# Performance work log

Measured on AMD Instinct MI355X. Metric: run time of the kernel, lower is better.

## Reference

```python
import jax, jax.numpy as jnp
import numpy as np

B, S, D, H = 2, 2048, 1024, 16
DK = D // H  # 64
NEG_FILL = -1e-08  # faithful to the original (NOT -1e9)


def setup_inputs() -> dict:
    key = jax.random.key(0)
    ks = jax.random.split(key, 11)
    init = 1.0 / np.sqrt(D)
    inp = {
        "Q": jax.random.normal(ks[0], (B, S, D), jnp.float32),
        "K": jax.random.normal(ks[1], (B, S, D), jnp.float32),
        "V": jax.random.normal(ks[2], (B, S, D), jnp.float32),
        # causal mask, broadcast over batch and heads
        "mask": jnp.tril(jnp.ones((1, 1, S, S), jnp.int32)),
        "Wq": jax.random.normal(ks[3], (D, D), jnp.float32) * init,
        "bq": jnp.zeros((D,), jnp.float32),
        "Wk": jax.random.normal(ks[4], (D, D), jnp.float32) * init,
        "bk": jnp.zeros((D,), jnp.float32),
        "Wv": jax.random.normal(ks[5], (D, D), jnp.float32) * init,
        "bv": jnp.zeros((D,), jnp.float32),
        "Wo": jax.random.normal(ks[6], (D, D), jnp.float32) * init,
        "bo": jnp.zeros((D,), jnp.float32),
    }
    return inp


def reference(Q, K, V, mask, Wq, bq, Wk, bk, Wv, bv, Wo, bo):
    # Linear projections (weights stored as [in, out]; same math as nn.Linear)
    q = Q @ Wq + bq  # [B,S,D]
    k = K @ Wk + bk
    v = V @ Wv + bv
    # split heads: [B,S,D] -> [B,H,S,DK]
    q = q.reshape(B, S, H, DK).transpose(0, 2, 1, 3)
    k = k.reshape(B, S, H, DK).transpose(0, 2, 1, 3)
    v = v.reshape(B, S, H, DK).transpose(0, 2, 1, 3)
    scores = jnp.einsum("bhqd,bhkd->bhqk", q, k) / np.sqrt(DK)  # [B,H,S,S]
    scores = jnp.where(mask == 0, NEG_FILL, scores)
    probs = jax.nn.softmax(scores, axis=-1)
    # dropout p=0.0 -> identity (deterministic baseline)
    ctx = jnp.einsum("bhqk,bhkd->bhqd", probs, v)  # [B,H,S,DK]
    ctx = ctx.transpose(0, 2, 1, 3).reshape(B, S, D)
    return ctx @ Wo + bo
```

## Files before the change

kernel.cpp:

```cpp
#include <hip/hip_runtime.h>
#include <hip/hip_bf16.h>
#include <stdint.h>
#include <math.h>

#define DI __device__ __forceinline__

typedef __bf16 bf16x8 __attribute__((ext_vector_type(8)));
typedef float f32x4 __attribute__((ext_vector_type(4)));
typedef unsigned short ushortx8 __attribute__((ext_vector_type(8)));

DI unsigned short f2bf(float f) {
    unsigned int u = __builtin_bit_cast(unsigned int, f);
    u += 0x7fffu + ((u >> 16) & 1u);
    return (unsigned short)(u >> 16);
}

DI unsigned int cvt_pk_bf16(float lo, float hi) {
    unsigned int r;
    asm("v_cvt_pk_bf16_f32 %0, %1, %2" : "=v"(r) : "v"(lo), "v"(hi));
    return r;
}

DI f32x4 mfma_16x16x32_bf16(bf16x8 a, bf16x8 b, f32x4 c) {
    return __builtin_amdgcn_mfma_f32_16x16x32_bf16(a, b, c, 0, 0, 0);
}

DI void gload16(const unsigned short* g, unsigned short* l) {
    __builtin_amdgcn_global_load_lds(
        (const __attribute__((address_space(1))) void*)g,
        (__attribute__((address_space(3))) void*)l, 16, 0, 0);
}

__global__ __launch_bounds__(256) void k_prep(
    const float* __restrict__ Q, const float* __restrict__ K, const float* __restrict__ V,
    unsigned short* __restrict__ qc, unsigned short* __restrict__ kc, unsigned short* __restrict__ vc,
    const float* __restrict__ w0, const float* __restrict__ w1,
    const float* __restrict__ w2, const float* __restrict__ w3,
    unsigned short* __restrict__ o0, unsigned short* __restrict__ o1,
    unsigned short* __restrict__ o2, unsigned short* __restrict__ o3)
{
    constexpr int N = 1024;
    __shared__ unsigned short L[64 * 64];
    const int bx = blockIdx.x;
    const int tid = threadIdx.x;

    if (bx < 3072) {
        const int z = bx >> 10;
        const int ib = bx & 1023;
        const float* s = z == 0 ? Q : z == 1 ? K : V;
        unsigned short* d = z == 0 ? qc : z == 1 ? kc : vc;
        const int i0 = ib * 256 + tid;
        #pragma unroll
        for (int it = 0; it < 4; ++it) {
            const int i = i0 + it * 262144;
            const float4 v = reinterpret_cast<const float4*>(s)[i];
            uint2 pk;
            pk.x = cvt_pk_bf16(v.x, v.y);
            pk.y = cvt_pk_bf16(v.z, v.w);
            reinterpret_cast<uint2*>(d)[i] = pk;
        }
    } else {
        const int r4 = bx - 3072;
        const int z = r4 >> 8;
        const int tile = r4 & 255;
        const float* W = z == 0 ? w0 : z == 1 ? w1 : z == 2 ? w2 : w3;
        unsigned short* O = z == 0 ? o0 : z == 1 ? o1 : z == 2 ? o2 : o3;
        const int k0 = (tile >> 4) * 64, n0 = (tile & 15) * 64;

        const int r = tid >> 2, cbase = (tid & 3) * 16;
        #pragma unroll
        for (int i = 0; i < 4; ++i) {
            const int c = cbase + i * 4;
            const float4 v = *reinterpret_cast<const float4*>(&W[(size_t)(k0 + r) * N + n0 + c]);
            uint2 pk;
            pk.x = cvt_pk_bf16(v.x, v.y);
            pk.y = cvt_pk_bf16(v.z, v.w);
            const int byte = r * 128 + ((c * 2) ^ ((r & 7) << 4));
            *reinterpret_cast<uint2*>(reinterpret_cast<char*>(L) + byte) = pk;
        }
        __syncthreads();

        const int n = tid >> 2, kc2 = (tid & 3) * 16;
        ushortx8 v0, v1;
        #pragma unroll
        for (int j = 0; j < 8; ++j) {
            const int ka = kc2 + j, kb2 = kc2 + 8 + j;
            v0[j] = *reinterpret_cast<const unsigned short*>(
                reinterpret_cast<const char*>(L) + ka * 128 + ((n * 2) ^ ((ka & 7) << 4)));
            v1[j] = *reinterpret_cast<const unsigned short*>(
                reinterpret_cast<const char*>(L) + kb2 * 128 + ((n * 2) ^ ((kb2 & 7) << 4)));
        }
        unsigned short* op = &O[(size_t)(n0 + n) * N + k0 + kc2];
        *reinterpret_cast<ushortx8*>(op) = v0;
        *reinterpret_cast<ushortx8*>(op + 8) = v1;
    }
}

template <int MODE, int BN>
__global__ __launch_bounds__(256) void k_gemm_bf16(
    const unsigned short* __restrict__ A0, const unsigned short* __restrict__ A1,
    const unsigned short* __restrict__ A2,
    const unsigned short* __restrict__ B0, const unsigned short* __restrict__ B1,
    const unsigned short* __restrict__ B2,
    const float* __restrict__ bias0, const float* __restrict__ bias1,
    const float* __restrict__ bias2,
    void* C0, void* C1, void* C2)
{
    constexpr int K = 1024, N = 1024;
    constexpr int NJ = BN / 32;
    const int z = MODE ? blockIdx.z : 0;
    const unsigned short* A  = z == 0 ? A0 : z == 1 ? A1 : A2;
    const unsigned short* Bt = z == 0 ? B0 : z == 1 ? B1 : B2;
    const float* bias        = z == 0 ? bias0 : z == 1 ? bias1 : bias2;
    void* C                  = z == 0 ? C0 : z == 1 ? C1 : C2;

    __shared__ unsigned short As[128 * 64];
    __shared__ unsigned short Bs[BN * 64];

    const int tid  = threadIdx.x;
    const int lane = tid & 63;
    const int w    = tid >> 6;
    const int wr   = w >> 1, wc = w & 1;
    const int fr   = lane & 15, kg = lane >> 4;
    const int m0   = blockIdx.x * 128, n0 = blockIdx.y * BN;

    const int srow8 = lane >> 3;
    const int sswz  = ((lane & 7) ^ (lane >> 3)) * 8;

    f32x4 acc[4][NJ] = {};

    for (int t = 0; t < K / 64; ++t) {
        const int k0 = t * 64;
        #pragma unroll
        for (int it = 0; it < 4; ++it) {
            const int c = w * 4 + it;
            gload16(&A[(size_t)(m0 + c * 8 + srow8) * K + k0 + sswz], &As[c * 512]);
            if (BN == 128)
                gload16(&Bt[(size_t)(n0 + c * 8 + srow8) * K + k0 + sswz], &Bs[c * 512]);
        }
        if (BN == 64) {
            #pragma unroll
            for (int it = 0; it < 2; ++it) {
                const int c = w * 2 + it;
                gload16(&Bt[(size_t)(n0 + c * 8 + srow8) * K + k0 + sswz], &Bs[c * 512]);
            }
        }
        __syncthreads();

        const int rsw = (fr & 7) << 4;
        #pragma unroll
        for (int kh = 0; kh < 2; ++kh) {
            bf16x8 af[4], bfj[NJ];
            #pragma unroll
            for (int i = 0; i < 4; ++i)
                af[i] = *reinterpret_cast<const bf16x8*>(
                    reinterpret_cast<const char*>(As) +
                    (wr * 64 + i * 16 + fr) * 128 + ((kh * 64 + kg * 16) ^ rsw));
            #pragma unroll
            for (int j = 0; j < NJ; ++j)
                bfj[j] = *reinterpret_cast<const bf16x8*>(
                    reinterpret_cast<const char*>(Bs) +
                    (wc * (BN / 2) + j * 16 + fr) * 128 + ((kh * 64 + kg * 16) ^ rsw));
            #pragma unroll
            for (int i = 0; i < 4; ++i)
                #pragma unroll
                for (int j = 0; j < NJ; ++j)
                    acc[i][j] = mfma_16x16x32_bf16(af[i], bfj[j], acc[i][j]);
        }
        __syncthreads();
    }

    if (MODE == 1 && z == 2) {
        unsigned short* vt = reinterpret_cast<unsigned short*>(C);
        #pragma unroll
        for (int i = 0; i < 4; ++i) {
            const int m = m0 + wr * 64 + i * 16 + kg * 4;
            const int bb = m >> 11, s = m & 2047;
            #pragma unroll
            for (int j = 0; j < NJ; ++j) {
                const int n = n0 + wc * (BN / 2) + j * 16 + fr;
                const float bv = bias[n];
                uint2 pk;
                pk.x = cvt_pk_bf16(acc[i][j][0] + bv, acc[i][j][1] + bv);
                pk.y = cvt_pk_bf16(acc[i][j][2] + bv, acc[i][j][3] + bv);
                *reinterpret_cast<uint2*>(&vt[((size_t)(bb * 1024 + n)) * 2048 + s]) = pk;
            }
        }
    } else if (MODE == 1) {
        const float sc = (z == 0) ? 0.125f * 1.44269504088896340736f : 1.0f;
        unsigned short* Cb = reinterpret_cast<unsigned short*>(C);
        #pragma unroll
        for (int i = 0; i < 4; ++i) {
            const int m = m0 + wr * 64 + i * 16 + kg * 4;
            #pragma unroll
            for (int j = 0; j < NJ; ++j) {
                const int n = n0 + wc * (BN / 2) + j * 16 + fr;
                const float bv = bias[n];
                const unsigned int p0 = cvt_pk_bf16((acc[i][j][0] + bv) * sc, (acc[i][j][1] + bv) * sc);
                const unsigned int p1 = cvt_pk_bf16((acc[i][j][2] + bv) * sc, (acc[i][j][3] + bv) * sc);
                Cb[(size_t)(m + 0) * N + n] = (unsigned short)p0;
                Cb[(size_t)(m + 1) * N + n] = (unsigned short)(p0 >> 16);
                Cb[(size_t)(m + 2) * N + n] = (unsigned short)p1;
                Cb[(size_t)(m + 3) * N + n] = (unsigned short)(p1 >> 16);
            }
        }
    } else {
        float* Cf = reinterpret_cast<float*>(C);
        #pragma unroll
        for (int i = 0; i < 4; ++i) {
            const int m = m0 + wr * 64 + i * 16 + kg * 4;
            #pragma unroll
            for (int j = 0; j < NJ; ++j) {
                const int n = n0 + wc * (BN / 2) + j * 16 + fr;
                const float bv = bias[n];
                #pragma unroll
                for (int r = 0; r < 4; ++r)
                    Cf[(size_t)(m + r) * N + n] = acc[i][j][r] + bv;
            }
        }
    }
}

__global__ __launch_bounds__(256) void k_vtail(
    const unsigned short* __restrict__ vt, float* __restrict__ vtail)
{
    const int row = blockIdx.x * 4 + (threadIdx.x >> 6);
    const int l = threadIdx.x & 63;
    const unsigned short* p = &vt[(size_t)row * 2048 + l * 32];
    float s = 0.f;
    #pragma unroll
    for (int i = 0; i < 4; ++i) {
        ushortx8 v = *reinterpret_cast<const ushortx8*>(&p[i * 8]);
        #pragma unroll
        for (int e = 0; e < 8; ++e)
            s += __builtin_bit_cast(float, (unsigned int)v[e] << 16);
    }
    #pragma unroll
    for (int off = 1; off < 64; off <<= 1) {
        const float t = __shfl_down(s, off, 64);
        s += (l + off < 64) ? t : 0.f;
    }
    float tv = __shfl(s, (2 * l + 2) & 63, 64);
    if (l == 31) tv = 0.f;
    if (l < 32) vtail[(size_t)row * 32 + l] = tv;
}

template <bool MASK>
DI void attn_tile(const unsigned char* KsB, const unsigned char* VtsB,
                  unsigned char* PB, bf16x8 qf0, bf16x8 qf1,
                  f32x4 (&o)[4], f32x4& oS, int w, int fr, int kg)
{
    const int sw = (fr & 7) << 4;
    #pragma unroll
    for (int j = 0; j < 4; ++j) {
        const int row = j * 16 + fr;
        const bf16x8 kf0 = *reinterpret_cast<const bf16x8*>(KsB + row * 128 + ((kg * 16) ^ sw));
        const bf16x8 kf1 = *reinterpret_cast<const bf16x8*>(KsB + row * 128 + ((64 + kg * 16) ^ sw));
        f32x4 s = {0.f, 0.f, 0.f, 0.f};
        __builtin_amdgcn_s_setprio(1);
        s = mfma_16x16x32_bf16(kf0, qf0, s);
        s = mfma_16x16x32_bf16(kf1, qf1, s);
        __builtin_amdgcn_s_setprio(0);
        float p[4];
        #pragma unroll
        for (int r = 0; r < 4; ++r) {
            float e = exp2f(s[r]);
            if (MASK && (j * 16 + kg * 4 + r > w * 16 + fr)) e = 1.0f;
            p[r] = e;
        }
        uint2 pk;
        pk.x = cvt_pk_bf16(p[0], p[1]);
        pk.y = cvt_pk_bf16(p[2], p[3]);
        *reinterpret_cast<uint2*>(PB + fr * 128 + ((j * 32 + kg * 8) ^ sw)) = pk;
    }
    bf16x8 ones;
    #pragma unroll
    for (int b = 0; b < 8; ++b) ones[b] = (__bf16)1.0f;
    __builtin_amdgcn_s_setprio(1);
    #pragma unroll
    for (int kk = 0; kk < 2; ++kk) {
        const bf16x8 pf = *reinterpret_cast<const bf16x8*>(PB + fr * 128 + ((kk * 64 + kg * 16) ^ sw));
        #pragma unroll
        for (int n = 0; n < 4; ++n) {
            const int vrow = n * 16 + fr;
            const bf16x8 vf = *reinterpret_cast<const bf16x8*>(VtsB + vrow * 128 + ((kk * 64 + kg * 16) ^ sw));
            o[n] = mfma_16x16x32_bf16(pf, vf, o[n]);
        }
        oS = mfma_16x16x32_bf16(pf, ones, oS);
    }
    __builtin_amdgcn_s_setprio(0);
}

DI void attn_sweep(int qt,
                   const unsigned short* __restrict__ qp,
                   const unsigned short* __restrict__ kp,
                   const unsigned short* __restrict__ vt,
                   const float* __restrict__ vtail,
                   unsigned short* __restrict__ ctx,
                   unsigned char (*KsB)[64 * 128], unsigned char (*VtsB)[64 * 128],
                   unsigned char* PB, size_t baseQ, size_t baseV, int b, int h,
                   int w, int fr, int kg, int sr, int sc8, int wb0, int wb1)
{
    constexpr int S = 2048, D = 1024;
    const int q0 = qt * 64 + w * 16;

    bf16x8 qf0, qf1;
    {
        const size_t roff = baseQ + (size_t)(q0 + fr) * D;
        qf0 = *reinterpret_cast<const bf16x8*>(&qp[roff + kg * 8]);
        qf1 = *reinterpret_cast<const bf16x8*>(&qp[roff + 32 + kg * 8]);
    }

    f32x4 o[4] = {};
    f32x4 oS = {};
    const int NT = qt + 1;

    {
        const ushortx8 kr0 = *reinterpret_cast<const ushortx8*>(&kp[baseQ + (size_t)sr * D + sc8]);
        const ushortx8 kr1 = *reinterpret_cast<const ushortx8*>(&kp[baseQ + (size_t)(sr + 32) * D + sc8]);
        const ushortx8 vr0 = *reinterpret_cast<const ushortx8*>(&vt[baseV + (size_t)sr * S + sc8]);
        const ushortx8 vr1 = *reinterpret_cast<const ushortx8*>(&vt[baseV + (size_t)(sr + 32) * S + sc8]);
        *reinterpret_cast<ushortx8*>(KsB[0] + wb0)  = kr0;
        *reinterpret_cast<ushortx8*>(KsB[0] + wb1)  = kr1;
        *reinterpret_cast<ushortx8*>(VtsB[0] + wb0) = vr0;
        *reinterpret_cast<ushortx8*>(VtsB[0] + wb1) = vr1;
    }
    __syncthreads();

    for (int t = 0; t < NT; ++t) {
        const int cur = t & 1;
        const bool more = (t + 1 < NT);
        ushortx8 nk0, nk1, nv0, nv1;
        if (more) {
            const int kt1 = (t + 1) * 64;
            nk0 = *reinterpret_cast<const ushortx8*>(&kp[baseQ + (size_t)(kt1 + sr) * D + sc8]);
            nk1 = *reinterpret_cast<const ushortx8*>(&kp[baseQ + (size_t)(kt1 + sr + 32) * D + sc8]);
            nv0 = *reinterpret_cast<const ushortx8*>(&vt[baseV + (size_t)sr * S + kt1 + sc8]);
            nv1 = *reinterpret_cast<const ushortx8*>(&vt[baseV + (size_t)(sr + 32) * S + kt1 + sc8]);
        }
        if (more)
            attn_tile<false>(KsB[cur], VtsB[cur], PB, qf0, qf1, o, oS, w, fr, kg);
        else
            attn_tile<true>(KsB[cur], VtsB[cur], PB, qf0, qf1, o, oS, w, fr, kg);
        if (more) {
            const int nxt = cur ^ 1;
            *reinterpret_cast<ushortx8*>(KsB[nxt] + wb0)  = nk0;
            *reinterpret_cast<ushortx8*>(KsB[nxt] + wb1)  = nk1;
            *reinterpret_cast<ushortx8*>(VtsB[nxt] + wb0) = nv0;
            *reinterpret_cast<ushortx8*>(VtsB[nxt] + wb1) = nv1;
        }
        __syncthreads();
    }

    const float tailc = (float)(S - (qt + 1) * 64);
    float rlq[4];
    #pragma unroll
    for (int r = 0; r < 4; ++r) rlq[r] = 1.0f / (oS[r] + tailc);

    float tl[4];
    #pragma unroll
    for (int n = 0; n < 4; ++n)
        tl[n] = vtail[((size_t)(b * 1024) + h * 64 + n * 16 + fr) * 32 + qt];

    #pragma unroll
    for (int n = 0; n < 4; ++n)
        #pragma unroll
        for (int r = 0; r < 4; ++r) {
            const int qrow = q0 + kg * 4 + r;
            ctx[baseQ + (size_t)qrow * D + n * 16 + fr] = f2bf((o[n][r] + tl[n]) * rlq[r]);
        }
}

__global__ __launch_bounds__(256, 2) void k_attn(
    const unsigned short* __restrict__ qp,
    const unsigned short* __restrict__ kp,
    const unsigned short* __restrict__ vt,
    const float* __restrict__ vtail,
    unsigned short* __restrict__ ctx)
{
    constexpr int S = 2048, D = 1024;
    const int L = blockIdx.x;
    const int G = (L & 7) * 64 + (L >> 3);
    const int p = G & 15;
    const int h = (G >> 4) & 15;
    const int b = G >> 8;

    __shared__ alignas(16) unsigned char KsB[2][64 * 128];
    __shared__ alignas(16) unsigned char VtsB[2][64 * 128];
    __shared__ alignas(16) unsigned char PlsB[4 * 16 * 128];

    const int tid  = threadIdx.x;
    const int lane = tid & 63, w = tid >> 6;
    const int fr   = lane & 15, kg = lane >> 4;
    unsigned char* PB = PlsB + w * 2048;

    const size_t baseQ = ((size_t)b * S) * D + (size_t)h * 64;
    const size_t baseV = ((size_t)b * D + (size_t)h * 64) * S;

    const int sr  = tid >> 3;
    const int sc8 = (tid & 7) * 8;
    const int wb0 = sr * 128 + (((tid & 7) * 16) ^ ((sr & 7) << 4));
    const int wb1 = (sr + 32) * 128 + (((tid & 7) * 16) ^ (((sr + 32) & 7) << 4));

    attn_sweep(31 - p, qp, kp, vt, vtail, ctx, KsB, VtsB, PB,
               baseQ, baseV, b, h, w, fr, kg, sr, sc8, wb0, wb1);
    attn_sweep(p, qp, kp, vt, vtail, ctx, KsB, VtsB, PB,
               baseQ, baseV, b, h, w, fr, kg, sr, sc8, wb0, wb1);
}

extern "C" void kernel_launch(void* const* d_in, const int* in_sizes, int n_in,
                              void* d_out, int out_size, void* d_ws, size_t ws_size,
                              hipStream_t stream) {
    constexpr int B = 2, S = 2048, D = 1024;
    constexpr int M = B * S;
    constexpr size_t MD = (size_t)M * D;

    const float* Q  = (const float*)d_in[0];
    const float* K  = (const float*)d_in[1];
    const float* V  = (const float*)d_in[2];
    const float* Wq = (const float*)d_in[4];
    const float* bq = (const float*)d_in[5];
    const float* Wk = (const float*)d_in[6];
    const float* bk = (const float*)d_in[7];
    const float* Wv = (const float*)d_in[8];
    const float* bv = (const float*)d_in[9];
    const float* Wo = (const float*)d_in[10];
    const float* bo = (const float*)d_in[11];

    unsigned short* qc = (unsigned short*)d_out;
    unsigned short* kc = qc + MD;
    char* ws = (char*)d_ws;
    unsigned short* qb  = (unsigned short*)(ws);
    unsigned short* kb  = (unsigned short*)(ws + (8u << 20));
    unsigned short* vtg = (unsigned short*)(ws + (16u << 20));
    unsigned short* vc  = (unsigned short*)(ws + (24u << 20));
    unsigned short* Wto = (unsigned short*)(ws + (32u << 20));
    unsigned short* Wtq = (unsigned short*)(ws + (34u << 20));
    unsigned short* Wtk = (unsigned short*)(ws + (36u << 20));
    unsigned short* Wtv = (unsigned short*)(ws + (38u << 20));
    unsigned short* ctx = vc;
    float* vtail        = (float*)Wtq;

    dim3 blk(256);
    k_prep<<<dim3(4096), blk, 0, stream>>>(
        Q, K, V, qc, kc, vc, Wq, Wk, Wv, Wo, Wtq, Wtk, Wtv, Wto);
    k_gemm_bf16<1, 64><<<dim3(M / 128, D / 64, 3), blk, 0, stream>>>(
        qc, kc, vc, Wtq, Wtk, Wtv, bq, bk, bv, qb, kb, vtg);
    k_vtail<<<dim3((B * D) / 4), blk, 0, stream>>>(vtg, vtail);
    k_attn<<<dim3(512), blk, 0, stream>>>(qb, kb, vtg, vtail, ctx);
    k_gemm_bf16<0, 64><<<dim3(M / 128, D / 64, 1), blk, 0, stream>>>(
        ctx, ctx, ctx, Wto, Wto, Wto, bo, bo, bo, d_out, d_out, d_out);
}
```

Baseline: 121.8 us.

## Stream K/V tiles directly into LDS with global-to-LDS loads; use native exp2

Replaces the register-staged K/V prefetch (global load to registers, then LDS store after compute) with direct global-to-LDS loads via a gload16 helper. The swizzle moves to the global-side column address so the data lands in the same XOR layout. This frees registers and removes the LDS store instructions from the loop. The exp2f call is also swapped for the hardware builtin. Correctness depends on gload16 already existing, on the swizzle mapping matching the reader's XOR pattern, and on __syncthreads waiting for the async LDS writes.

```diff
diff --git a/kernel.cpp b/kernel.cpp
--- a/kernel.cpp
+++ b/kernel.cpp
@@ -264,7 +264,7 @@
         float p[4];
         #pragma unroll
         for (int r = 0; r < 4; ++r) {
-            float e = exp2f(s[r]);
+            float e = __builtin_amdgcn_exp2f(s[r]);
             if (MASK && (j * 16 + kg * 4 + r > w * 16 + fr)) e = 1.0f;
             p[r] = e;
         }
@@ -299,7 +299,7 @@
                    unsigned short* __restrict__ ctx,
                    unsigned char (*KsB)[64 * 128], unsigned char (*VtsB)[64 * 128],
                    unsigned char* PB, size_t baseQ, size_t baseV, int b, int h,
-                   int w, int fr, int kg, int sr, int sc8, int wb0, int wb1)
+                   int lane, int w, int fr, int kg)
 {
     constexpr int S = 2048, D = 1024;
     const int q0 = qt * 64 + w * 16;
@@ -315,40 +315,39 @@
     f32x4 oS = {};
     const int NT = qt + 1;
 
-    {
-        const ushortx8 kr0 = *reinterpret_cast<const ushortx8*>(&kp[baseQ + (size_t)sr * D + sc8]);
-        const ushortx8 kr1 = *reinterpret_cast<const ushortx8*>(&kp[baseQ + (size_t)(sr + 32) * D + sc8]);
-        const ushortx8 vr0 = *reinterpret_cast<const ushortx8*>(&vt[baseV + (size_t)sr * S + sc8]);
-        const ushortx8 vr1 = *reinterpret_cast<const ushortx8*>(&vt[baseV + (size_t)(sr + 32) * S + sc8]);
-        *reinterpret_cast<ushortx8*>(KsB[0] + wb0)  = kr0;
-        *reinterpret_cast<ushortx8*>(KsB[0] + wb1)  = kr1;
-        *reinterpret_cast<ushortx8*>(VtsB[0] + wb0) = vr0;
-        *reinterpret_cast<ushortx8*>(VtsB[0] + wb1) = vr1;
+    const int srow = lane >> 3;
+    const int sswz = ((lane & 7) ^ srow) * 8;
+    const int c0   = w * 2;
+
+    #pragma unroll
+    for (int i = 0; i < 2; ++i) {
+        const int c = c0 + i;
+        const int row = c * 8 + srow;
+        gload16(&kp[baseQ + (size_t)row * D + sswz],
+                reinterpret_cast<unsigned short*>(KsB[0] + c * 1024));
+        gload16(&vt[baseV + (size_t)row * S + sswz],
+                reinterpret_cast<unsigned short*>(VtsB[0] + c * 1024));
     }
     __syncthreads();
 
     for (int t = 0; t < NT; ++t) {
         const int cur = t & 1;
-        const bool more = (t + 1 < NT);
-        ushortx8 nk0, nk1, nv0, nv1;
-        if (more) {
+        if (t + 1 < NT) {
             const int kt1 = (t + 1) * 64;
-            nk0 = *reinterpret_cast<const ushortx8*>(&kp[baseQ + (size_t)(kt1 + sr) * D + sc8]);
-            nk1 = *reinterpret_cast<const ushortx8*>(&kp[baseQ + (size_t)(kt1 + sr + 32) * D + sc8]);
-            nv0 = *reinterpret_cast<const ushortx8*>(&vt[baseV + (size_t)sr * S + kt1 + sc8]);
-            nv1 = *reinterpret_cast<const ushortx8*>(&vt[baseV + (size_t)(sr + 32) * S + kt1 + sc8]);
-        }
-        if (more)
+            #pragma unroll
+            for (int i = 0; i < 2; ++i) {
+                const int c = c0 + i;
+                const int row = c * 8 + srow;
+                gload16(&kp[baseQ + (size_t)(kt1 + row) * D + sswz],
+                        reinterpret_cast<unsigned short*>(KsB[cur ^ 1] + c * 1024));
+                gload16(&vt[baseV + (size_t)row * S + kt1 + sswz],
+                        reinterpret_cast<unsigned short*>(VtsB[cur ^ 1] + c * 1024));
+            }
+        }
+        if (t == NT - 1)
+            attn_tile<true>(KsB[cur], VtsB[cur], PB, qf0, qf1, o, oS, w, fr, kg);
+        else
             attn_tile<false>(KsB[cur], VtsB[cur], PB, qf0, qf1, o, oS, w, fr, kg);
-        else
-            attn_tile<true>(KsB[cur], VtsB[cur], PB, qf0, qf1, o, oS, w, fr, kg);
-        if (more) {
-            const int nxt = cur ^ 1;
-            *reinterpret_cast<ushortx8*>(KsB[nxt] + wb0)  = nk0;
-            *reinterpret_cast<ushortx8*>(KsB[nxt] + wb1)  = nk1;
-            *reinterpret_cast<ushortx8*>(VtsB[nxt] + wb0) = nv0;
-            *reinterpret_cast<ushortx8*>(VtsB[nxt] + wb1) = nv1;
-        }
         __syncthreads();
     }
 
@@ -397,15 +396,10 @@
     const size_t baseQ = ((size_t)b * S) * D + (size_t)h * 64;
     const size_t baseV = ((size_t)b * D + (size_t)h * 64) * S;
 
-    const int sr  = tid >> 3;
-    const int sc8 = (tid & 7) * 8;
-    const int wb0 = sr * 128 + (((tid & 7) * 16) ^ ((sr & 7) << 4));
-    const int wb1 = (sr + 32) * 128 + (((tid & 7) * 16) ^ (((sr + 32) & 7) << 4));
-
     attn_sweep(31 - p, qp, kp, vt, vtail, ctx, KsB, VtsB, PB,
-               baseQ, baseV, b, h, w, fr, kg, sr, sc8, wb0, wb1);
+               baseQ, baseV, b, h, lane, w, fr, kg);
     attn_sweep(p, qp, kp, vt, vtail, ctx, KsB, VtsB, PB,
-               baseQ, baseV, b, h, w, fr, kg, sr, sc8, wb0, wb1);
+               baseQ, baseV, b, h, lane, w, fr, kg);
 }
 
 extern "C" void kernel_launch(void* const* d_in, const int* in_sizes, int n_in,
```

After: 117.8 us. 3.3% less time.
